# Optimization experiments

Hardware: AMD Instinct MI355X
Metric: run time of the kernel (lower is better)

## Reference

```python
import jax, jax.numpy as jnp
import numpy as np

# lanes: [WL, WT, EL, ET, NL, NT, SL, ST] -> indices 0..7
# phase -> its two start lanes (standard FRAP 8-phase mapping)
PHASE_LANES = np.array([[1, 3], [5, 7], [0, 2], [4, 6], [0, 1], [2, 3], [4, 5], [6, 7]])
NUM_PHASE = 8
# ordered (i, j) pairs with i != j, nested-loop (row-major) order as in torch code
_PI, _PJ = np.where(~np.eye(NUM_PHASE, dtype=bool))


def _conv1x1(w, b, x):
    # w: [O, C], b: [O], x: [B, C, H, W] -> [B, O, H, W]
    return jnp.einsum('oc,bchw->bohw', w, x) + b[:, None, None]


def setup_inputs() -> dict:
    key = jax.random.key(0)
    ks = jax.random.split(key, 16)
    B = 16384
    phase_bits = jax.random.randint(ks[0], (B, 8), 0, 2).astype(jnp.float32)
    veh_counts = jax.random.randint(ks[1], (B, 8), 0, 30).astype(jnp.float32)
    feature_input = jnp.concatenate([phase_bits, veh_counts], axis=1)  # [B, 16]
    constant_mask = jax.random.randint(ks[2], (1, 8, 7), 0, 2)          # [1, 8, 7]
    s = 0.1
    return {
        'feature_input': feature_input,
        'emb_phase': jax.random.normal(ks[3], (2, 4)) * s,
        'w_veh': jax.random.normal(ks[4], (4,)) * s,   # Linear(1,4) weight
        'b_veh': jax.random.normal(ks[5], (4,)) * s,
        'w_line': jax.random.normal(ks[6], (16, 8)) * s,
        'b_line': jax.random.normal(ks[7], (16,)) * s,
        'emb_const': jax.random.normal(ks[8], (2, 4)) * s,
        'w_feat': jax.random.normal(ks[9], (20, 32)) * s,
        'b_feat': jax.random.normal(ks[10], (20,)) * s,
        'w_const': jax.random.normal(ks[11], (20, 4)) * s,
        'b_const': jax.random.normal(ks[12], (20,)) * s,
        'w_comb': jax.random.normal(ks[13], (20, 20)) * s,
        'b_comb': jax.random.normal(ks[14], (20,)) * s,
        'w_final': jax.random.normal(ks[15], (1, 20)) * s,
        'b_final': jnp.zeros((1,)),
        'constant_mask': constant_mask,
    }


def reference(feature_input, emb_phase, w_veh, b_veh, w_line, b_line, emb_const,
              w_feat, b_feat, w_const, b_const, w_comb, b_comb, w_final, b_final,
              constant_mask):
    B = feature_input.shape[0]
    phase_idx = feature_input[:, :8].astype(jnp.int32)          # [B, 8]
    veh = feature_input[:, 8:]                                   # [B, 8]
    fp = jax.nn.sigmoid(emb_phase[phase_idx])                    # [B, 8, 4]
    fv = jax.nn.sigmoid(veh[..., None] * w_veh + b_veh)          # [B, 8, 4]
    lines = jnp.concatenate([fv, fp], axis=-1)                   # [B, 8, 8]
    x = jax.nn.relu(jnp.einsum('bld,od->blo', lines, w_line) + b_line)  # [B, 8, 16]
    pressure = x[:, PHASE_LANES].sum(axis=2)                     # [B, 8, 16]
    # pairwise concat, pair-major stacking then reshape (faithful to torch cat/reshape)
    con = jnp.concatenate([pressure[:, _PI], pressure[:, _PJ]], axis=-1)  # [B, 56, 32]
    fm = jnp.transpose(con, (1, 0, 2)).reshape(B, NUM_PHASE, NUM_PHASE - 1, 32)
    fm = jnp.transpose(fm, (0, 3, 1, 2))                         # [B, 32, 8, 7]
    cm = emb_const[constant_mask]                                # [1, 8, 7, 4]
    cm = jnp.transpose(cm, (0, 3, 1, 2))                         # [1, 4, 8, 7]
    xf = jax.nn.relu(_conv1x1(w_feat, b_feat, fm))               # [B, 20, 8, 7]
    yc = jax.nn.relu(_conv1x1(w_const, b_const, cm))             # [1, 20, 8, 7]
    z = xf * yc
    z = jax.nn.relu(_conv1x1(w_comb, b_comb, z))                 # [B, 20, 8, 7]
    z = jax.nn.relu(_conv1x1(w_final, b_final, z))               # [B, 1, 8, 7]
    z = z.sum(axis=-1).reshape(-1, NUM_PHASE)                    # [B, 8]
    return z
```

## Files before the change

### kernel.cpp

```cpp
#include <hip/hip_runtime.h>
#include <hip/hip_bf16.h>

__device__ __forceinline__ float sigm(float x) { return 1.0f / (1.0f + __expf(-x)); }

#define WS_WCM   0
#define WS_YA    800
#define WS_YB    2000
#define WS_BCOMB 3200
#define WS_WFIN  3220
#define WS_BFIN  3240

__global__ __launch_bounds__(256) void frap_setup(
    const float* __restrict__ emb_phase, const float* __restrict__ w_veh,
    const float* __restrict__ b_veh,     const float* __restrict__ w_line,
    const float* __restrict__ b_line,    const float* __restrict__ emb_const,
    const float* __restrict__ w_feat,    const float* __restrict__ b_feat,
    const float* __restrict__ w_const,   const float* __restrict__ b_const,
    const float* __restrict__ w_comb,    const float* __restrict__ b_comb,
    const float* __restrict__ w_final,   const float* __restrict__ b_final,
    float* __restrict__ ws)
{
    __shared__ float s_stage[820];
    const int tid = threadIdx.x;
    for (int k = tid; k < 128; k += 256) s_stage[k] = w_line[k];
    for (int k = tid; k < 640; k += 256) s_stage[128 + k] = w_feat[k];
    if (tid < 16)                s_stage[768 + tid] = b_line[tid];
    if (tid < 4)                 s_stage[784 + tid] = w_veh[tid];
    if (tid >= 4 && tid < 8)     s_stage[784 + tid] = b_veh[tid - 4];
    if (tid >= 8 && tid < 16)    s_stage[784 + tid] = emb_phase[tid - 8];
    if (tid >= 16 && tid < 36)   s_stage[784 + tid] = b_feat[tid - 16];
    __syncthreads();

    if (tid < 240) {
        int key = tid >> 2, part = tid & 3;
        int veh = key >> 1, pb = key & 1;
        float vf = (float)veh;
        float line[8];
#pragma unroll
        for (int k = 0; k < 4; k++) line[k] = sigm(fmaf(vf, s_stage[784 + k], s_stage[788 + k]));
#pragma unroll
        for (int k = 0; k < 4; k++) line[4 + k] = sigm(s_stage[792 + pb * 4 + k]);
        float X[16];
#pragma unroll
        for (int o = 0; o < 16; o++) {
            float x = s_stage[768 + o];
#pragma unroll
            for (int d = 0; d < 8; d++) x = fmaf(line[d], s_stage[o * 8 + d], x);
            X[o] = fmaxf(x, 0.f);
        }
        int o0 = part * 5;
#pragma unroll
        for (int oo = 0; oo < 5; oo++) {
            int o = o0 + oo;
            float a = 0.25f * s_stage[800 + o];
            float bb = a;
#pragma unroll
            for (int c = 0; c < 16; c++) {
                a  = fmaf(X[c], s_stage[128 + o * 32 + c], a);
                bb = fmaf(X[c], s_stage[128 + o * 32 + 16 + c], bb);
            }
            ws[WS_YA + key * 20 + o] = a;
            ws[WS_YB + key * 20 + o] = bb;
        }
    }

    for (int idx = tid; idx < 800; idx += 256) {
        int m = idx / 400;
        int r = idx - m * 400;
        int q = r / 20;
        int o = r - q * 20;
        float yc = b_const[o];
#pragma unroll
        for (int k = 0; k < 4; k++)
            yc = fmaf(w_const[o * 4 + k], emb_const[m * 4 + k], yc);
        ws[WS_WCM + idx] = w_comb[q * 20 + o] * fmaxf(yc, 0.f);
    }
    if (tid < 20) { ws[WS_BCOMB + tid] = b_comb[tid]; ws[WS_WFIN + tid] = w_final[tid]; }
    if (tid == 0) ws[WS_BFIN] = b_final[0];
}

__global__ __launch_bounds__(448, 4) void frap_main(
    const float* __restrict__ feat, const int* __restrict__ cmask,
    const float* __restrict__ ws, float* __restrict__ out, int B)
{
    __shared__ __align__(16) float s_y[2400];
    __shared__ float s_part[448];

    const int tid = threadIdx.x;
    for (int k = tid; k < 600; k += 448)
        ((float4*)s_y)[k] = ((const float4*)(ws + WS_YA))[k];

    const int i = blockIdx.x & 7;
    const int chunk = blockIdx.x >> 3;
    const int lane = tid & 63;
    const int jw = __builtin_amdgcn_readfirstlane(tid >> 6);
    const int bp = (chunk << 6) + lane;
    const bool valid = bp < B;
    const int bpc = valid ? bp : 0;

    const int mbit = __builtin_amdgcn_readfirstlane(cmask[i * 7 + jw]) & 1;
    const float* wbase = ws + WS_WCM + (mbit ? 400 : 0);
    __syncthreads();

    const unsigned Bu = (unsigned)B;
    unsigned g = 56u * (unsigned)bpc + 7u * (unsigned)i + (unsigned)jw;
    unsigned p = g / Bu;
    unsigned b = g - p * Bu;
    unsigned pi = p / 7u;
    unsigned c7 = p - pi * 7u;
    unsigned pj = c7 + (c7 >= pi ? 1u : 0u);

    const unsigned L0T = 0x64204051u, L1T = 0x75316273u;
    int la0 = (L0T >> (pi * 4)) & 15, la1 = (L1T >> (pi * 4)) & 15;
    int lb0 = (L0T >> (pj * 4)) & 15, lb1 = (L1T >> (pj * 4)) & 15;

    const float* row = feat + (size_t)b * 16;
    float bA0 = row[la0], vA0 = row[8 + la0];
    float bA1 = row[la1], vA1 = row[8 + la1];
    float bB0 = row[lb0], vB0 = row[8 + lb0];
    float bB1 = row[lb1], vB1 = row[8 + lb1];
    int kA0 = min(59, max(0, (int)fmaf(vA0, 2.f, bA0)));
    int kA1 = min(59, max(0, (int)fmaf(vA1, 2.f, bA1)));
    int kB0 = min(59, max(0, (int)fmaf(vB0, 2.f, bB0)));
    int kB1 = min(59, max(0, (int)fmaf(vB1, 2.f, bB1)));

    const float4* A0 = (const float4*)(s_y + kA0 * 20);
    const float4* A1 = (const float4*)(s_y + kA1 * 20);
    const float4* B0 = (const float4*)(s_y + 1200 + kB0 * 20);
    const float4* B1 = (const float4*)(s_y + 1200 + kB1 * 20);

    float xf[20];
#pragma unroll
    for (int r = 0; r < 5; r++) {
        float4 a0 = A0[r], a1 = A1[r], c0 = B0[r], c1 = B1[r];
        xf[4 * r + 0] = fmaxf(a0.x + a1.x + c0.x + c1.x, 0.f);
        xf[4 * r + 1] = fmaxf(a0.y + a1.y + c0.y + c1.y, 0.f);
        xf[4 * r + 2] = fmaxf(a0.z + a1.z + c0.z + c1.z, 0.f);
        xf[4 * r + 3] = fmaxf(a0.w + a1.w + c0.w + c1.w, 0.f);
    }

    float acc = 0.f;
    for (int q = 0; q < 20; q++) {
        const float4* wr = (const float4*)(wbase + q * 20);
        float4 w0 = wr[0], w1 = wr[1], w2 = wr[2], w3 = wr[3], w4 = wr[4];
        float h = ws[WS_BCOMB + q];
        h = fmaf(w0.x, xf[0],  h); h = fmaf(w0.y, xf[1],  h);
        h = fmaf(w0.z, xf[2],  h); h = fmaf(w0.w, xf[3],  h);
        h = fmaf(w1.x, xf[4],  h); h = fmaf(w1.y, xf[5],  h);
        h = fmaf(w1.z, xf[6],  h); h = fmaf(w1.w, xf[7],  h);
        h = fmaf(w2.x, xf[8],  h); h = fmaf(w2.y, xf[9],  h);
        h = fmaf(w2.z, xf[10], h); h = fmaf(w2.w, xf[11], h);
        h = fmaf(w3.x, xf[12], h); h = fmaf(w3.y, xf[13], h);
        h = fmaf(w3.z, xf[14], h); h = fmaf(w3.w, xf[15], h);
        h = fmaf(w4.x, xf[16], h); h = fmaf(w4.y, xf[17], h);
        h = fmaf(w4.z, xf[18], h); h = fmaf(w4.w, xf[19], h);
        acc = fmaf(ws[WS_WFIN + q], fmaxf(h, 0.f), acc);
    }
    float val = fmaxf(acc + ws[WS_BFIN], 0.f);

    s_part[tid] = val;
    __syncthreads();
    if (jw == 0 && valid) {
        float total = val;
#pragma unroll
        for (int w = 1; w < 7; w++)
            total += s_part[lane + (w << 6)];
        out[(size_t)bp * 8 + i] = total;
    }
}

extern "C" void kernel_launch(void* const* d_in, const int* in_sizes, int n_in,
                              void* d_out, int out_size, void* d_ws, size_t ws_size,
                              hipStream_t stream) {
    const float* feat      = (const float*)d_in[0];
    const float* emb_phase = (const float*)d_in[1];
    const float* w_veh     = (const float*)d_in[2];
    const float* b_veh     = (const float*)d_in[3];
    const float* w_line    = (const float*)d_in[4];
    const float* b_line    = (const float*)d_in[5];
    const float* emb_const = (const float*)d_in[6];
    const float* w_feat    = (const float*)d_in[7];
    const float* b_feat    = (const float*)d_in[8];
    const float* w_const   = (const float*)d_in[9];
    const float* b_const   = (const float*)d_in[10];
    const float* w_comb    = (const float*)d_in[11];
    const float* b_comb    = (const float*)d_in[12];
    const float* w_final   = (const float*)d_in[13];
    const float* b_final   = (const float*)d_in[14];
    const int*   cmask     = (const int*)d_in[15];

    int B = in_sizes[0] / 16;
    float* ws = (float*)d_ws;

    frap_setup<<<1, 256, 0, stream>>>(emb_phase, w_veh, b_veh, w_line, b_line,
                                      emb_const, w_feat, b_feat, w_const,
                                      b_const, w_comb, b_comb, w_final,
                                      b_final, ws);
    int blocks = 8 * ((B + 63) / 64);
    frap_main<<<blocks, 448, 0, stream>>>(feat, cmask, ws, (float*)d_out, B);
}
```

Before: 113.2 us.

## Precompute packed per-pair lookup indices in setup kernel for coalesced main reads

Adds extra blocks to the setup kernel that compute, for each (pair, batch) element, the four clamped table indices and pack them into one 32-bit word laid out so the main kernel reads them contiguously by flattened index. The main kernel drops its scattered reads of the feature rows and its integer divisions, replacing them with one coalesced 4-byte load. This adds a full extra pass writing 56*B words and reading the features, plus a kernel dependency. It also assumes B is a multiple of 256, and padded threads in the last main chunk read index zero.

```diff
diff --git a/kernel.cpp b/kernel.cpp
--- a/kernel.cpp
+++ b/kernel.cpp
@@ -9,8 +9,10 @@
 #define WS_BCOMB 3200
 #define WS_WFIN  3220
 #define WS_BFIN  3240
-
-__global__ __launch_bounds__(256) void frap_setup(
+#define WS_KP    4096
+
+__global__ __launch_bounds__(256) void frap_setup_all(
+    const float* __restrict__ feat,
     const float* __restrict__ emb_phase, const float* __restrict__ w_veh,
     const float* __restrict__ b_veh,     const float* __restrict__ w_line,
     const float* __restrict__ b_line,    const float* __restrict__ emb_const,
@@ -18,10 +20,32 @@
     const float* __restrict__ w_const,   const float* __restrict__ b_const,
     const float* __restrict__ w_comb,    const float* __restrict__ b_comb,
     const float* __restrict__ w_final,   const float* __restrict__ b_final,
-    float* __restrict__ ws)
+    float* __restrict__ ws, int B, int nkp)
 {
+    const int tid = threadIdx.x;
+    const unsigned L0T = 0x64204051u, L1T = 0x75316273u;
+
+    if ((int)blockIdx.x < nkp) {
+        const int bpp = B >> 8;
+        const int p = blockIdx.x / bpp;
+        const int b = (blockIdx.x - p * bpp) * 256 + tid;
+        unsigned pi = (unsigned)p / 7u;
+        unsigned c7 = (unsigned)p - pi * 7u;
+        unsigned pj = c7 + (c7 >= pi ? 1u : 0u);
+        int la0 = (L0T >> (pi * 4)) & 15, la1 = (L1T >> (pi * 4)) & 15;
+        int lb0 = (L0T >> (pj * 4)) & 15, lb1 = (L1T >> (pj * 4)) & 15;
+        const float* row = feat + (size_t)b * 16;
+        int kA0 = min(59, max(0, (int)fmaf(row[8 + la0], 2.f, row[la0])));
+        int kA1 = min(59, max(0, (int)fmaf(row[8 + la1], 2.f, row[la1])));
+        int kB0 = min(59, max(0, (int)fmaf(row[8 + lb0], 2.f, row[lb0])));
+        int kB1 = min(59, max(0, (int)fmaf(row[8 + lb1], 2.f, row[lb1])));
+        unsigned kp = (unsigned)kA0 | ((unsigned)kA1 << 8) |
+                      ((unsigned)kB0 << 16) | ((unsigned)kB1 << 24);
+        ((unsigned*)ws)[WS_KP + (size_t)p * B + b] = kp;
+        return;
+    }
+
     __shared__ float s_stage[820];
-    const int tid = threadIdx.x;
     for (int k = tid; k < 128; k += 256) s_stage[k] = w_line[k];
     for (int k = tid; k < 640; k += 256) s_stage[128 + k] = w_feat[k];
     if (tid < 16)                s_stage[768 + tid] = b_line[tid];
@@ -80,7 +104,7 @@
 }
 
 __global__ __launch_bounds__(448, 4) void frap_main(
-    const float* __restrict__ feat, const int* __restrict__ cmask,
+    const int* __restrict__ cmask,
     const float* __restrict__ ws, float* __restrict__ out, int B)
 {
     __shared__ __align__(16) float s_y[2400];
@@ -102,27 +126,10 @@
     const float* wbase = ws + WS_WCM + (mbit ? 400 : 0);
     __syncthreads();
 
-    const unsigned Bu = (unsigned)B;
-    unsigned g = 56u * (unsigned)bpc + 7u * (unsigned)i + (unsigned)jw;
-    unsigned p = g / Bu;
-    unsigned b = g - p * Bu;
-    unsigned pi = p / 7u;
-    unsigned c7 = p - pi * 7u;
-    unsigned pj = c7 + (c7 >= pi ? 1u : 0u);
-
-    const unsigned L0T = 0x64204051u, L1T = 0x75316273u;
-    int la0 = (L0T >> (pi * 4)) & 15, la1 = (L1T >> (pi * 4)) & 15;
-    int lb0 = (L0T >> (pj * 4)) & 15, lb1 = (L1T >> (pj * 4)) & 15;
-
-    const float* row = feat + (size_t)b * 16;
-    float bA0 = row[la0], vA0 = row[8 + la0];
-    float bA1 = row[la1], vA1 = row[8 + la1];
-    float bB0 = row[lb0], vB0 = row[8 + lb0];
-    float bB1 = row[lb1], vB1 = row[8 + lb1];
-    int kA0 = min(59, max(0, (int)fmaf(vA0, 2.f, bA0)));
-    int kA1 = min(59, max(0, (int)fmaf(vA1, 2.f, bA1)));
-    int kB0 = min(59, max(0, (int)fmaf(vB0, 2.f, bB0)));
-    int kB1 = min(59, max(0, (int)fmaf(vB1, 2.f, bB1)));
+    const unsigned g = 56u * (unsigned)bpc + 7u * (unsigned)i + (unsigned)jw;
+    const unsigned kp = ((const unsigned*)ws)[WS_KP + g];
+    const int kA0 = kp & 255, kA1 = (kp >> 8) & 255;
+    const int kB0 = (kp >> 16) & 255, kB1 = (kp >> 24) & 255;
 
     const float4* A0 = (const float4*)(s_y + kA0 * 20);
     const float4* A1 = (const float4*)(s_y + kA1 * 20);
@@ -192,10 +199,12 @@
     int B = in_sizes[0] / 16;
     float* ws = (float*)d_ws;
 
-    frap_setup<<<1, 256, 0, stream>>>(emb_phase, w_veh, b_veh, w_line, b_line,
-                                      emb_const, w_feat, b_feat, w_const,
-                                      b_const, w_comb, b_comb, w_final,
-                                      b_final, ws);
+    int nkp = 56 * (B >> 8);
+    frap_setup_all<<<nkp + 1, 256, 0, stream>>>(feat, emb_phase, w_veh, b_veh,
+                                                w_line, b_line, emb_const,
+                                                w_feat, b_feat, w_const,
+                                                b_const, w_comb, b_comb,
+                                                w_final, b_final, ws, B, nkp);
     int blocks = 8 * ((B + 63) / 64);
-    frap_main<<<blocks, 448, 0, stream>>>(feat, cmask, ws, (float*)d_out, B);
+    frap_main<<<blocks, 448, 0, stream>>>(cmask, ws, (float*)d_out, B);
 }
```

Measured after the change: 123.5 us. 9.1% more time.
